# Performance work log

Hardware: AMD Instinct MI355X
Metric: run time of the kernel (lower is better)

Reference implementation:

```python
import jax, jax.numpy as jnp
import numpy as np

N_NODES = 25000
N_EDGES = 400000
N_GRAPHS = 64
F_IN = 128


def setup_inputs() -> dict:
    key = jax.random.key(0)
    ks = jax.random.split(key, 16)
    inp = {}
    inp["x"] = jax.random.normal(ks[0], (N_NODES, F_IN), dtype=jnp.float32)
    inp["edge_index"] = jax.random.randint(ks[1], (2, N_EDGES), 0, N_NODES, dtype=jnp.int64)
    inp["edge_attr"] = jax.random.uniform(ks[2], (N_EDGES,), dtype=jnp.float32)
    inp["batch_ids"] = jnp.sort(jax.random.randint(ks[3], (N_NODES,), 0, N_GRAPHS, dtype=jnp.int64))
    def lin(k, fan_in, fan_out):
        bound = 1.0 / np.sqrt(fan_in)
        return jax.random.uniform(k, (fan_in, fan_out), dtype=jnp.float32, minval=-bound, maxval=bound)
    inp["W1_rel"] = lin(ks[4], F_IN, 512)
    inp["b1"] = jnp.zeros((512,), jnp.float32)
    inp["W1_root"] = lin(ks[5], F_IN, 512)
    inp["W2_rel"] = lin(ks[6], 512, 512)
    inp["b2"] = jnp.zeros((512,), jnp.float32)
    inp["W2_root"] = lin(ks[7], 512, 512)
    inp["Wl1"] = lin(ks[8], 512, 64)
    inp["bl1"] = jnp.zeros((64,), jnp.float32)
    inp["Wl2"] = lin(ks[9], 64, 16)
    inp["bl2"] = jnp.zeros((16,), jnp.float32)
    inp["Wl3"] = lin(ks[10], 16, 1)
    inp["bl3"] = jnp.zeros((1,), jnp.float32)
    return inp


def _graph_conv(h, src, dst, edge_attr, W_rel, b_rel, W_root, n_nodes):
    # PyG GraphConv: lin_rel(scatter_add(w_e * x_src, dst)) + lin_root(x)
    msg = h[src] * edge_attr[:, None]                       # [E, F] gather
    agg = jax.ops.segment_sum(msg, dst, num_segments=n_nodes)  # [N, F] scatter-add
    return agg @ W_rel + b_rel + h @ W_root


def reference(x, edge_index, edge_attr, batch_ids, W1_rel, b1, W1_root,
              W2_rel, b2, W2_root, Wl1, bl1, Wl2, bl2, Wl3, bl3):
    n_nodes = x.shape[0]
    src, dst = edge_index[0], edge_index[1]
    h = jax.nn.relu(_graph_conv(x, src, dst, edge_attr, W1_rel, b1, W1_root, n_nodes))
    h = jax.nn.relu(_graph_conv(h, src, dst, edge_attr, W2_rel, b2, W2_root, n_nodes))
    # global mean pool by graph id
    sums = jax.ops.segment_sum(h, batch_ids, num_segments=N_GRAPHS)  # [G, 512]
    counts = jax.ops.segment_sum(jnp.ones((n_nodes,), h.dtype), batch_ids, num_segments=N_GRAPHS)
    g = sums / jnp.maximum(counts, 1.0)[:, None]
    # dropout is identity in eval mode
    g = jax.nn.relu(g @ Wl1 + bl1)
    g = jax.nn.relu(g @ Wl2 + bl2)
    return g @ Wl3 + bl3  # [G, 1]
```

## Files before the change

### kernel.cpp

```cpp
#include <hip/hip_runtime.h>
#include <hip/hip_bf16.h>
#include <hip/hip_fp16.h>
#include <stdint.h>

#define N_NODESC 25000
#define N_EDGESC 400000
#define N_GRAPHSC 64
#define F_INC 128
#define HIDC 512
#define PSTRIDE 1600000

typedef __attribute__((ext_vector_type(8))) short short8;
typedef __attribute__((ext_vector_type(8))) _Float16 half8;
typedef __attribute__((ext_vector_type(4))) float f32x4;

__device__ __forceinline__ unsigned short f2h(float f) {
  return __half_as_ushort(__float2half_rn(f));
}

__global__ __launch_bounds__(256)
void prep_kernel(const float* __restrict__ x, const int* __restrict__ ei,
                 const float* __restrict__ W1rel, const float* __restrict__ W1root,
                 const float* __restrict__ W2rel, const float* __restrict__ W2root,
                 unsigned short* __restrict__ xp, unsigned short* __restrict__ W1T,
                 unsigned short* __restrict__ W2T, int* __restrict__ deg,
                 float* __restrict__ gsum) {
  int blk = blockIdx.x, t = threadIdx.x;
  if (blk < 1563) {
    int e = blk * 256 + t;
    if (e < N_EDGESC) atomicAdd(&deg[ei[N_EDGESC + e]], 1);
  } else if (blk < 4688) {
    int idx = ((blk - 1563) * 256 + t) * 4;
    int node = idx >> 7;
    int col = idx & 127;
    float4 v = *(const float4*)(x + idx);
    ushort4 o;
    o.x = f2h(v.x); o.y = f2h(v.y); o.z = f2h(v.z); o.w = f2h(v.w);
    *(ushort4*)(xp + (size_t)(col >> 6) * PSTRIDE + (size_t)node * 64 + (col & 63)) = o;
  } else if (blk < 4848) {
    __shared__ float tile[64][65];
    int b2 = blk - 4688;
    const float* src;
    unsigned short* dst;
    int n0, k0, Kout;
    if (b2 < 128) {
      int kt = b2 >> 3, nt = b2 & 7;
      k0 = kt * 64; n0 = nt * 64;
      src = (k0 < 512) ? (W2rel + (size_t)k0 * 512) : (W2root + (size_t)(k0 - 512) * 512);
      dst = W2T; Kout = 1024;
    } else {
      int b = b2 - 128;
      int kt = b >> 3, nt = b & 7;
      k0 = kt * 64; n0 = nt * 64;
      src = (k0 < 128) ? (W1rel + (size_t)k0 * 512) : (W1root + (size_t)(k0 - 128) * 512);
      dst = W1T; Kout = 256;
    }
    int c = t & 63;
    int r4 = t >> 6;
#pragma unroll
    for (int rr = 0; rr < 64; rr += 4) {
      int row = rr + r4;
      tile[c][row] = src[(size_t)row * 512 + n0 + c];
    }
    __syncthreads();
#pragma unroll
    for (int rr = 0; rr < 64; rr += 4) {
      int nrow = rr + r4;
      dst[(size_t)(n0 + nrow) * Kout + k0 + c] = f2h(tile[nrow][c]);
    }
  } else {
    int i = (blk - 4848) * 256 + t;
    if (i < N_GRAPHSC * HIDC) gsum[i] = 0.f;
  }
}

__global__ __launch_bounds__(1024)
void scan_kernel(const int* __restrict__ deg, int* __restrict__ indptr, int* __restrict__ cursor,
                 int* __restrict__ sorted) {
  __shared__ int sums[1024];
  __shared__ int binsS[1024];
  __shared__ int scan2[1024];
  const int t = threadIdx.x;
  const int CH = (N_NODESC + 1023) / 1024;
  const int base = t * CH;
  const unsigned ub = (unsigned)deg[N_NODESC];
  const int stripe = t & 3;
  binsS[t] = 0;
  __syncthreads();
  int dl[CH];
  int s = 0;
  for (int i = 0; i < CH; ++i) {
    int idx = base + i;
    int d = (idx < N_NODESC) ? (int)((unsigned)deg[idx] - ub) : -1;
    dl[i] = d;
    if (d >= 0) {
      s += d;
      atomicAdd(&binsS[(d > 255 ? 255 : d) * 4 + stripe], 1);
    }
  }
  sums[t] = s;
  __syncthreads();
  int bv = binsS[t];
  scan2[t] = bv;
  __syncthreads();
  for (int off = 1; off < 1024; off <<= 1) {
    int v1 = (t >= off) ? sums[t - off] : 0;
    int v2 = (t >= off) ? scan2[t - off] : 0;
    __syncthreads();
    sums[t] += v1;
    scan2[t] += v2;
    __syncthreads();
  }
  binsS[t] = scan2[t] - bv;
  __syncthreads();
  int run = (t > 0) ? sums[t - 1] : 0;
  for (int i = 0; i < CH; ++i) {
    int idx = base + i;
    if (idx < N_NODESC) {
      indptr[idx] = run;
      cursor[idx] = run;
      run += dl[i];
      int fb = (dl[i] > 255 ? 255 : dl[i]) * 4 + stripe;
      int pos = atomicAdd(&binsS[fb], 1);
      sorted[pos] = idx;
    }
  }
  if (t == 0) indptr[N_NODESC] = sums[1023];
}

__global__ void fill_kernel(const int* __restrict__ ei, const float* __restrict__ ea,
                            int* __restrict__ cursor, unsigned* __restrict__ emeta) {
  int e = blockIdx.x * blockDim.x + threadIdx.x;
  if (e >= N_EDGESC) return;
  int dst = ei[N_EDGESC + e];
  int pos = atomicAdd(&cursor[dst], 1);
  unsigned short hw = __half_as_ushort(__float2half_rn(ea[e]));
  emeta[pos] = (unsigned)ei[e] | ((unsigned)hw << 16);
}

__global__ __launch_bounds__(256)
void agg_gather_s(const unsigned short* __restrict__ feat, const int* __restrict__ indptr,
                  const unsigned* __restrict__ emeta, const int* __restrict__ sorted,
                  unsigned short* __restrict__ outp, int lgP) {
  int panel = blockIdx.x & ((1 << lgP) - 1);
  int nidx = (blockIdx.x >> lgP) * 32 + (threadIdx.x >> 3);
  if (nidx >= N_NODESC) return;
  int c8 = threadIdx.x & 7;
  int node = sorted[nidx];
  int beg = indptr[node];
  int deg = indptr[node + 1] - beg;
  const unsigned* mp = emeta + beg;
  const char* fb = (const char*)(feat + (size_t)panel * PSTRIDE);
  unsigned coff = c8 * 16u;
  float acc0[8] = {}, acc1[8] = {};
  int j = 0;
  for (; j + 8 <= deg; j += 8) {
    unsigned m[8];
    half8 v[8];
    float w[8];
#pragma unroll
    for (int q = 0; q < 8; ++q) m[q] = mp[j + q];
#pragma unroll
    for (int q = 0; q < 8; ++q) v[q] = *(const half8*)(fb + (m[q] & 0xffffu) * 128u + coff);
#pragma unroll
    for (int q = 0; q < 8; ++q) w[q] = __half2float(__ushort_as_half((unsigned short)(m[q] >> 16)));
#pragma unroll
    for (int q = 0; q < 8; ++q) {
      if (q & 1) {
#pragma unroll
        for (int c = 0; c < 8; ++c) acc1[c] += (float)v[q][c] * w[q];
      } else {
#pragma unroll
        for (int c = 0; c < 8; ++c) acc0[c] += (float)v[q][c] * w[q];
      }
    }
  }
  if (j + 4 <= deg) {
    unsigned m0_ = mp[j], m1_ = mp[j + 1], m2_ = mp[j + 2], m3_ = mp[j + 3];
    half8 v0 = *(const half8*)(fb + (m0_ & 0xffffu) * 128u + coff);
    half8 v1 = *(const half8*)(fb + (m1_ & 0xffffu) * 128u + coff);
    half8 v2 = *(const half8*)(fb + (m2_ & 0xffffu) * 128u + coff);
    half8 v3 = *(const half8*)(fb + (m3_ & 0xffffu) * 128u + coff);
    float w0 = __half2float(__ushort_as_half((unsigned short)(m0_ >> 16)));
    float w1 = __half2float(__ushort_as_half((unsigned short)(m1_ >> 16)));
    float w2 = __half2float(__ushort_as_half((unsigned short)(m2_ >> 16)));
    float w3 = __half2float(__ushort_as_half((unsigned short)(m3_ >> 16)));
#pragma unroll
    for (int c = 0; c < 8; ++c) acc0[c] += (float)v0[c] * w0;
#pragma unroll
    for (int c = 0; c < 8; ++c) acc1[c] += (float)v1[c] * w1;
#pragma unroll
    for (int c = 0; c < 8; ++c) acc0[c] += (float)v2[c] * w2;
#pragma unroll
    for (int c = 0; c < 8; ++c) acc1[c] += (float)v3[c] * w3;
    j += 4;
  }
  if (j + 2 <= deg) {
    unsigned mA = mp[j], mB = mp[j + 1];
    half8 vA = *(const half8*)(fb + (mA & 0xffffu) * 128u + coff);
    half8 vB = *(const half8*)(fb + (mB & 0xffffu) * 128u + coff);
    float wA = __half2float(__ushort_as_half((unsigned short)(mA >> 16)));
    float wB = __half2float(__ushort_as_half((unsigned short)(mB >> 16)));
#pragma unroll
    for (int c = 0; c < 8; ++c) acc0[c] += (float)vA[c] * wA;
#pragma unroll
    for (int c = 0; c < 8; ++c) acc1[c] += (float)vB[c] * wB;
    j += 2;
  }
  if (j < deg) {
    unsigned mA = mp[j];
    half8 vA = *(const half8*)(fb + (mA & 0xffffu) * 128u + coff);
    float wA = __half2float(__ushort_as_half((unsigned short)(mA >> 16)));
#pragma unroll
    for (int c = 0; c < 8; ++c) acc0[c] += (float)vA[c] * wA;
  }
  half8 o;
#pragma unroll
  for (int c = 0; c < 8; ++c) o[c] = (_Float16)(acc0[c] + acc1[c]);
  *(half8*)(outp + (size_t)panel * PSTRIDE + (size_t)node * 64 + c8 * 8) = o;
}

__device__ __forceinline__ void gemm_map3(int b, int& m0, int& n0) {
  int g = (b & 7) * 98 + (b >> 3);
  m0 = (g >> 2) << 7;
  n0 = (g & 3) << 7;
}

__device__ __forceinline__ void stage_a(const short* Apan, int m0, int M,
                                        short* dst, int wave, int lane) {
#pragma unroll
  for (int i = 0; i < 4; ++i) {
    int s = ((i * 4 + wave) << 6) + lane;
    int row = s >> 3;
    int c = (s & 7) ^ (row & 7);
    int rg = m0 + row;
    if (rg > M - 1) rg = M - 1;
    const short* gp = Apan + (size_t)rg * 64 + (c << 3);
    __builtin_amdgcn_global_load_lds(
        (const __attribute__((address_space(1))) void*)gp,
        (__attribute__((address_space(3))) void*)(dst + ((i * 4 + wave) << 9)),
        16, 0, 0);
  }
}

__device__ __forceinline__ void stage_b(const short* BT, int n0, int K, int kbase,
                                        short* dst, int wave, int lane) {
#pragma unroll
  for (int i = 0; i < 4; ++i) {
    int s = ((i * 4 + wave) << 6) + lane;
    int row = s >> 3;
    int c = (s & 7) ^ (row & 7);
    const short* gp = BT + (size_t)(n0 + row) * K + kbase + (c << 3);
    __builtin_amdgcn_global_load_lds(
        (const __attribute__((address_space(1))) void*)gp,
        (__attribute__((address_space(3))) void*)(dst + ((i * 4 + wave) << 9)),
        16, 0, 0);
  }
}

__device__ __forceinline__ const short* apan_sel(const short* A0, const short* A1,
                                                 int S, int kt) {
  int kb = kt << 6;
  const short* Ab = (kb < S) ? A0 : A1;
  int koff = (kb < S) ? kb : kb - S;
  return Ab + (size_t)(koff >> 6) * PSTRIDE;
}

__device__ __forceinline__ void wg_barrier() {
  asm volatile("" ::: "memory");
  __builtin_amdgcn_s_barrier();
  asm volatile("" ::: "memory");
}

__device__ __forceinline__ void gemm_core(const short* A0, const short* A1,
                                          const short* BT, int M, int S,
                                          int m0, int n0, short* As, short* Bs,
                                          f32x4 (&acc)[4][4]) {
  const int K = 2 * S;
  const int nk = K >> 6;
  const int tid = threadIdx.x;
  const int wave = tid >> 6;
  const int lane = tid & 63;
  const int quad = lane >> 4;
  const int r = lane & 15;
  const int wm = (wave >> 1) << 6;
  const int wn = (wave & 1) << 6;

  int aoff[2][4], boff[2][4];
#pragma unroll
  for (int p = 0; p < 2; ++p) {
#pragma unroll
    for (int tm = 0; tm < 4; ++tm) {
      int ml = wm + tm * 16 + r;
      int c = (p << 2) + quad;
      aoff[p][tm] = (ml * 8 + (c ^ (ml & 7))) * 8;
    }
#pragma unroll
    for (int tn = 0; tn < 4; ++tn) {
      int nl = wn + tn * 16 + r;
      int c = (p << 2) + quad;
      boff[p][tn] = (nl * 8 + (c ^ (nl & 7))) * 8;
    }
  }

  stage_a(apan_sel(A0, A1, S, 0), m0, M, As, wave, lane);
  stage_b(BT, n0, K, 0, Bs, wave, lane);
  asm volatile("s_waitcnt vmcnt(0)");
  wg_barrier();

  for (int t = 0; t < nk; ++t) {
    const int cur = t & 1;
    const int nxt = cur ^ 1;
    int kt1 = (t + 1 < nk) ? t + 1 : nk - 1;
    stage_a(apan_sel(A0, A1, S, kt1), m0, M, As + nxt * 8192, wave, lane);
    stage_b(BT, n0, K, kt1 << 6, Bs + nxt * 8192, wave, lane);

    const short* Ac = As + cur * 8192;
    const short* Bc = Bs + cur * 8192;
    {
      half8 af[4], bf[4];
#pragma unroll
      for (int tm = 0; tm < 4; ++tm) af[tm] = *(const half8*)&Ac[aoff[0][tm]];
#pragma unroll
      for (int tn = 0; tn < 4; ++tn) bf[tn] = *(const half8*)&Bc[boff[0][tn]];
      __builtin_amdgcn_s_setprio(1);
#pragma unroll
      for (int tm = 0; tm < 4; ++tm)
#pragma unroll
        for (int tn = 0; tn < 4; ++tn)
          acc[tm][tn] = __builtin_amdgcn_mfma_f32_16x16x32_f16(af[tm], bf[tn], acc[tm][tn], 0, 0, 0);
      __builtin_amdgcn_s_setprio(0);
    }
    {
      half8 af[4], bf[4];
#pragma unroll
      for (int tm = 0; tm < 4; ++tm) af[tm] = *(const half8*)&Ac[aoff[1][tm]];
#pragma unroll
      for (int tn = 0; tn < 4; ++tn) bf[tn] = *(const half8*)&Bc[boff[1][tn]];
      __builtin_amdgcn_s_setprio(1);
#pragma unroll
      for (int tm = 0; tm < 4; ++tm)
#pragma unroll
        for (int tn = 0; tn < 4; ++tn)
          acc[tm][tn] = __builtin_amdgcn_mfma_f32_16x16x32_f16(af[tm], bf[tn], acc[tm][tn], 0, 0, 0);
      __builtin_amdgcn_s_setprio(0);
    }
    asm volatile("s_waitcnt vmcnt(0)");
    wg_barrier();
  }
}

__global__ __launch_bounds__(256, 2)
void gemm_bt_relu(const short* __restrict__ A0, const short* __restrict__ A1,
                  const short* __restrict__ BT, const float* __restrict__ bias,
                  unsigned short* __restrict__ Outp, int M, int S) {
  __shared__ __align__(16) short As[2 * 8192];
  __shared__ __align__(16) short Bs[2 * 8192];
  int m0, n0;
  gemm_map3(blockIdx.x, m0, n0);
  const int wave = threadIdx.x >> 6;
  const int lane = threadIdx.x & 63;
  const int quad = lane >> 4;
  const int r = lane & 15;
  const int wm = (wave >> 1) << 6;
  const int wn = (wave & 1) << 6;

  f32x4 acc[4][4] = {};
  gemm_core(A0, A1, BT, M, S, m0, n0, As, Bs, acc);

#pragma unroll
  for (int tm = 0; tm < 4; ++tm) {
    int rowb = m0 + wm + tm * 16 + quad * 4;
#pragma unroll
    for (int tn = 0; tn < 4; ++tn) {
      int col = n0 + wn + tn * 16 + r;
      float bv = bias[col];
      unsigned short* obase = Outp + (size_t)(col >> 6) * PSTRIDE + (col & 63);
#pragma unroll
      for (int reg = 0; reg < 4; ++reg) {
        int rr = rowb + reg;
        if (rr < M) {
          float v = acc[tm][tn][reg] + bv;
          v = v > 0.f ? v : 0.f;
          obase[(size_t)rr * 64] = f2h(v);
        }
      }
    }
  }
}

__global__ __launch_bounds__(256, 2)
void gemm_bt_pool(const short* __restrict__ A0, const short* __restrict__ A1,
                  const short* __restrict__ BT, const float* __restrict__ bias,
                  const int* __restrict__ batch, float* __restrict__ gsum, int M, int S) {
  __shared__ __align__(16) short As[2 * 8192];
  __shared__ __align__(16) short Bs[2 * 8192];
  int m0, n0;
  gemm_map3(blockIdx.x, m0, n0);
  const int wave = threadIdx.x >> 6;
  const int lane = threadIdx.x & 63;
  const int quad = lane >> 4;
  const int r = lane & 15;
  const int wm = (wave >> 1) << 6;
  const int wn = (wave & 1) << 6;

  f32x4 acc[4][4] = {};
  gemm_core(A0, A1, BT, M, S, m0, n0, As, Bs, acc);

  int gid[4][4];
#pragma unroll
  for (int tm = 0; tm < 4; ++tm) {
    int rowb = m0 + wm + tm * 16 + quad * 4;
#pragma unroll
    for (int reg = 0; reg < 4; ++reg) {
      int rr = rowb + reg;
      gid[tm][reg] = batch[rr < M ? rr : (M - 1)];
    }
#pragma unroll
    for (int tn = 0; tn < 4; ++tn) {
      float bv = bias[n0 + wn + tn * 16 + r];
#pragma unroll
      for (int reg = 0; reg < 4; ++reg) {
        int rr = rowb + reg;
        float v = acc[tm][tn][reg] + bv;
        v = v > 0.f ? v : 0.f;
        acc[tm][tn][reg] = (rr < M) ? v : 0.f;
      }
    }
  }
  int g_lo = batch[m0 < M ? m0 : (M - 1)];
  int g_hi = batch[(m0 + 127) < M ? (m0 + 127) : (M - 1)];
  for (int g = g_lo; g <= g_hi; ++g) {
#pragma unroll
    for (int tn = 0; tn < 4; ++tn) {
      float s = 0.f;
#pragma unroll
      for (int tm = 0; tm < 4; ++tm)
#pragma unroll
        for (int reg = 0; reg < 4; ++reg)
          s += (gid[tm][reg] == g) ? acc[tm][tn][reg] : 0.f;
      s += __shfl_xor(s, 16);
      s += __shfl_xor(s, 32);
      if (quad == 0)
        atomicAdd(&gsum[(size_t)g * HIDC + n0 + wn + tn * 16 + r], s);
    }
  }
}

__global__ __launch_bounds__(256)
void mlp_kernel(const float* __restrict__ gsum, const int* __restrict__ batch,
                const float* __restrict__ Wl1, const float* __restrict__ bl1,
                const float* __restrict__ Wl2, const float* __restrict__ bl2,
                const float* __restrict__ Wl3, const float* __restrict__ bl3,
                float* __restrict__ out) {
  int gi = blockIdx.x;
  int t = threadIdx.x;
  int unit = t & 63;
  int part = t >> 6;
  __shared__ float red[4][64];
  __shared__ float h1s[64];
  __shared__ float h2s[16];
  int lo = 0, hi = N_NODESC;
  while (lo < hi) { int mid = (lo + hi) >> 1; if (batch[mid] < gi) lo = mid + 1; else hi = mid; }
  int start = lo;
  hi = N_NODESC;
  while (lo < hi) { int mid = (lo + hi) >> 1; if (batch[mid] < gi + 1) lo = mid + 1; else hi = mid; }
  float inv = 1.0f / fmaxf((float)(lo - start), 1.0f);
  const float* gr = gsum + gi * HIDC;
  float acc = 0.f;
  for (int j = part * 128; j < (part + 1) * 128; ++j)
    acc += gr[j] * Wl1[j * 64 + unit];
  red[part][unit] = acc;
  __syncthreads();
  if (t < 64) {
    float a = bl1[t] + (red[0][t] + red[1][t] + red[2][t] + red[3][t]) * inv;
    h1s[t] = fmaxf(a, 0.f);
  }
  __syncthreads();
  if (t < 16) {
    float a = bl2[t];
    for (int j = 0; j < 64; ++j) a += h1s[j] * Wl2[j * 16 + t];
    h2s[t] = fmaxf(a, 0.f);
  }
  __syncthreads();
  if (t == 0) {
    float a = bl3[0];
    for (int j = 0; j < 16; ++j) a += h2s[j] * Wl3[j];
    out[gi] = a;
  }
}

extern "C" void kernel_launch(void* const* d_in, const int* in_sizes, int n_in,
                              void* d_out, int out_size, void* d_ws, size_t ws_size,
                              hipStream_t stream) {
  const float* x      = (const float*)d_in[0];
  const int*   ei     = (const int*)d_in[1];
  const float* ea     = (const float*)d_in[2];
  const int*   batch  = (const int*)d_in[3];
  const float* W1rel  = (const float*)d_in[4];
  const float* b1     = (const float*)d_in[5];
  const float* W1root = (const float*)d_in[6];
  const float* W2rel  = (const float*)d_in[7];
  const float* b2     = (const float*)d_in[8];
  const float* W2root = (const float*)d_in[9];
  const float* Wl1    = (const float*)d_in[10];
  const float* bl1    = (const float*)d_in[11];
  const float* Wl2    = (const float*)d_in[12];
  const float* bl2    = (const float*)d_in[13];
  const float* Wl3    = (const float*)d_in[14];
  const float* bl3    = (const float*)d_in[15];
  float* out = (float*)d_out;

  char* ws = (char*)d_ws;
  unsigned short* xp     = (unsigned short*)(ws + 0);
  unsigned short* agg1p  = (unsigned short*)(ws + 6400000);
  unsigned short* h1p    = (unsigned short*)(ws + 12800000);
  unsigned short* agg2p  = (unsigned short*)(ws + 38400000);
  unsigned short* W1T    = (unsigned short*)(ws + 64000000);
  unsigned short* W2T    = (unsigned short*)(ws + 64262144);
  float*          gsum   = (float*)(ws + 65310720);
  int*            deg    = (int*)(ws + 65441792);
  int*            cursor = (int*)(ws + 65541796);
  int*            indptr = (int*)(ws + 65641796);
  unsigned*       emeta  = (unsigned*)(ws + 65741812);
  int*            sorted = (int*)(ws + 67341812);

  prep_kernel<<<4976, 256, 0, stream>>>(x, ei, W1rel, W1root, W2rel, W2root,
                                        xp, W1T, W2T, deg, gsum);
  scan_kernel<<<1, 1024, 0, stream>>>(deg, indptr, cursor, sorted);
  fill_kernel<<<(N_EDGESC + 255) / 256, 256, 0, stream>>>(ei, ea, cursor, emeta);

  const int NBLK = (N_NODESC + 31) / 32;
  agg_gather_s<<<NBLK * 2, 256, 0, stream>>>(xp, indptr, emeta, sorted, agg1p, 1);

  gemm_bt_relu<<<784, 256, 0, stream>>>((const short*)agg1p, (const short*)xp,
                                        (const short*)W1T, b1, h1p, N_NODESC, 128);

  agg_gather_s<<<NBLK * 8, 256, 0, stream>>>(h1p, indptr, emeta, sorted, agg2p, 3);

  gemm_bt_pool<<<784, 256, 0, stream>>>((const short*)agg2p, (const short*)h1p,
                                        (const short*)W2T, b2, batch, gsum, N_NODESC, 512);

  mlp_kernel<<<N_GRAPHSC, 256, 0, stream>>>(gsum, batch, Wl1, bl1, Wl2, bl2, Wl3, bl3, out);
}
```

Before: 307.6 us.

## Use wave-shuffle scans in CSR build and shrink gather unroll to 4

The single-block scan kernel now assigns nodes to waves in strided, coalesced order and computes prefix sums with wave shuffles plus a 16-wave scan, instead of per-thread contiguous chunks and a 1024-wide shared-memory scan. This targets the serial per-thread loop and uncoalesced degree loads in the CSR construction. Separately, the aggregation gather loop drops its 8-edge unroll in favour of a 4-edge main loop, which lowers register pressure but leaves fewer loads in flight per thread.

```diff
diff --git a/kernel.cpp b/kernel.cpp
--- a/kernel.cpp
+++ b/kernel.cpp
@@ -77,55 +77,82 @@
 __global__ __launch_bounds__(1024)
 void scan_kernel(const int* __restrict__ deg, int* __restrict__ indptr, int* __restrict__ cursor,
                  int* __restrict__ sorted) {
-  __shared__ int sums[1024];
   __shared__ int binsS[1024];
   __shared__ int scan2[1024];
+  __shared__ int Wsh[16];
+  __shared__ int waveBase[16];
+  __shared__ int gTot;
   const int t = threadIdx.x;
-  const int CH = (N_NODESC + 1023) / 1024;
-  const int base = t * CH;
+  const int w = t >> 6;
+  const int lane = t & 63;
+  const int stripe = t & 3;
+  const int nbase = w * 1600;
   const unsigned ub = (unsigned)deg[N_NODESC];
-  const int stripe = t & 3;
   binsS[t] = 0;
   __syncthreads();
-  int dl[CH];
-  int s = 0;
-  for (int i = 0; i < CH; ++i) {
-    int idx = base + i;
-    int d = (idx < N_NODESC) ? (int)((unsigned)deg[idx] - ub) : -1;
+
+  int dl[25];
+  int tw = 0;
+#pragma unroll
+  for (int i = 0; i < 25; ++i) {
+    int idx = nbase + i * 64 + lane;
+    int d = (idx < N_NODESC) ? (int)((unsigned)deg[idx] - ub) : 0;
     dl[i] = d;
-    if (d >= 0) {
-      s += d;
+    if (idx < N_NODESC) {
+      tw += d;
       atomicAdd(&binsS[(d > 255 ? 255 : d) * 4 + stripe], 1);
     }
   }
-  sums[t] = s;
-  __syncthreads();
+#pragma unroll
+  for (int off = 32; off > 0; off >>= 1) tw += __shfl_xor(tw, off);
+  if (lane == 0) Wsh[w] = tw;
+  __syncthreads();
+
+  if (t < 16) {
+    int v = Wsh[t];
+    int s = v;
+#pragma unroll
+    for (int off = 1; off < 16; off <<= 1) {
+      int u = __shfl_up(s, off);
+      if (t >= off) s += u;
+    }
+    waveBase[t] = s - v;
+    if (t == 15) gTot = s;
+  }
   int bv = binsS[t];
   scan2[t] = bv;
   __syncthreads();
   for (int off = 1; off < 1024; off <<= 1) {
-    int v1 = (t >= off) ? sums[t - off] : 0;
     int v2 = (t >= off) ? scan2[t - off] : 0;
     __syncthreads();
-    sums[t] += v1;
     scan2[t] += v2;
     __syncthreads();
   }
   binsS[t] = scan2[t] - bv;
   __syncthreads();
-  int run = (t > 0) ? sums[t - 1] : 0;
-  for (int i = 0; i < CH; ++i) {
-    int idx = base + i;
+
+  int run = waveBase[w];
+#pragma unroll
+  for (int i = 0; i < 25; ++i) {
+    int idx = nbase + i * 64 + lane;
+    int d = dl[i];
+    int s = d;
+#pragma unroll
+    for (int off = 1; off < 64; off <<= 1) {
+      int u = __shfl_up(s, off);
+      if (lane >= off) s += u;
+    }
+    int excl = run + s - d;
     if (idx < N_NODESC) {
-      indptr[idx] = run;
-      cursor[idx] = run;
-      run += dl[i];
-      int fb = (dl[i] > 255 ? 255 : dl[i]) * 4 + stripe;
+      indptr[idx] = excl;
+      cursor[idx] = excl;
+      int fb = (d > 255 ? 255 : d) * 4 + stripe;
       int pos = atomicAdd(&binsS[fb], 1);
       sorted[pos] = idx;
     }
-  }
-  if (t == 0) indptr[N_NODESC] = sums[1023];
+    run += __shfl(s, 63);
+  }
+  if (t == 0) indptr[N_NODESC] = gTot;
 }
 
 __global__ void fill_kernel(const int* __restrict__ ei, const float* __restrict__ ea,
@@ -154,29 +181,11 @@
   unsigned coff = c8 * 16u;
   float acc0[8] = {}, acc1[8] = {};
   int j = 0;
-  for (; j + 8 <= deg; j += 8) {
-    unsigned m[8];
-    half8 v[8];
-    float w[8];
-#pragma unroll
-    for (int q = 0; q < 8; ++q) m[q] = mp[j + q];
-#pragma unroll
-    for (int q = 0; q < 8; ++q) v[q] = *(const half8*)(fb + (m[q] & 0xffffu) * 128u + coff);
-#pragma unroll
-    for (int q = 0; q < 8; ++q) w[q] = __half2float(__ushort_as_half((unsigned short)(m[q] >> 16)));
-#pragma unroll
-    for (int q = 0; q < 8; ++q) {
-      if (q & 1) {
-#pragma unroll
-        for (int c = 0; c < 8; ++c) acc1[c] += (float)v[q][c] * w[q];
-      } else {
-#pragma unroll
-        for (int c = 0; c < 8; ++c) acc0[c] += (float)v[q][c] * w[q];
-      }
-    }
-  }
-  if (j + 4 <= deg) {
-    unsigned m0_ = mp[j], m1_ = mp[j + 1], m2_ = mp[j + 2], m3_ = mp[j + 3];
+  for (; j + 4 <= deg; j += 4) {
+    unsigned m0_ = mp[j];
+    unsigned m1_ = mp[j + 1];
+    unsigned m2_ = mp[j + 2];
+    unsigned m3_ = mp[j + 3];
     half8 v0 = *(const half8*)(fb + (m0_ & 0xffffu) * 128u + coff);
     half8 v1 = *(const half8*)(fb + (m1_ & 0xffffu) * 128u + coff);
     half8 v2 = *(const half8*)(fb + (m2_ & 0xffffu) * 128u + coff);
@@ -193,10 +202,10 @@
     for (int c = 0; c < 8; ++c) acc0[c] += (float)v2[c] * w2;
 #pragma unroll
     for (int c = 0; c < 8; ++c) acc1[c] += (float)v3[c] * w3;
-    j += 4;
   }
   if (j + 2 <= deg) {
-    unsigned mA = mp[j], mB = mp[j + 1];
+    unsigned mA = mp[j];
+    unsigned mB = mp[j + 1];
     half8 vA = *(const half8*)(fb + (mA & 0xffffu) * 128u + coff);
     half8 vB = *(const half8*)(fb + (mB & 0xffffu) * 128u + coff);
     float wA = __half2float(__ushort_as_half((unsigned short)(mA >> 16)));
```

Result: faster. 285.3 us (-7.3%).
